# Kernel optimization log

Hardware: AMD Instinct MI355X
Metric: run time of the kernel (lower is better)

Reference implementation:

```python
import jax, jax.numpy as jnp
import numpy as np

N = 50000        # nodes
E = 640000       # edges
HID = 128        # hidden_channels
HEADS = 2
C = HID // 2     # out_channels per head (64)
ATT_SLOPE = 0.2  # GATv2Conv leaky_relu slope
OUT_SLOPE = 0.01 # F.leaky_relu default slope in GAT.forward


def setup_inputs() -> dict:
    key = jax.random.key(0)
    ks = jax.random.split(key, 11)
    s = 0.05
    return {
        "x": jax.random.normal(ks[0], (N, HID), dtype=jnp.float32),
        "edge_index": jax.random.randint(ks[1], (2, E), 0, N, dtype=jnp.int32),
        # layer 1 params (torch Linear layout: [out, in])
        "w_l1": jax.random.normal(ks[2], (HEADS * C, HID), dtype=jnp.float32) * s,
        "w_r1": jax.random.normal(ks[3], (HEADS * C, HID), dtype=jnp.float32) * s,
        "att1": jax.random.normal(ks[4], (HEADS, C), dtype=jnp.float32) * s,
        "b1": jnp.zeros((HEADS * C,), dtype=jnp.float32),
        # layer 2 params
        "w_l2": jax.random.normal(ks[5], (HEADS * C, HID), dtype=jnp.float32) * s,
        "w_r2": jax.random.normal(ks[6], (HEADS * C, HID), dtype=jnp.float32) * s,
        "att2": jax.random.normal(ks[7], (HEADS, C), dtype=jnp.float32) * s,
        "b2": jnp.zeros((HEADS * C,), dtype=jnp.float32),
    }


def gatv2_conv(x, src, dst, w_l, w_r, att, b):
    # x: [N, HID] -> out: [N, HEADS*C]  (concat=True), dropout inactive (eval)
    x_l = (x @ w_l.T).reshape(N, HEADS, C)  # source transform
    x_r = (x @ w_r.T).reshape(N, HEADS, C)  # target transform
    x_j = x_l[src]                           # [E, H, C] gathered source feats
    e = jax.nn.leaky_relu(x_j + x_r[dst], ATT_SLOPE)
    alpha = jnp.einsum('ehc,hc->eh', e, att)  # [E, H]
    # segment softmax over incoming edges of each target node
    amax = jax.ops.segment_max(alpha, dst, num_segments=N)
    amax = jnp.where(jnp.isfinite(amax), amax, 0.0)
    ex = jnp.exp(alpha - amax[dst])
    denom = jax.ops.segment_sum(ex, dst, num_segments=N)
    alpha = ex / (denom[dst] + 1e-16)
    out = jax.ops.segment_sum(alpha[:, :, None] * x_j, dst, num_segments=N)
    return out.reshape(N, HEADS * C) + b


def reference(x, edge_index, w_l1, w_r1, att1, b1, w_l2, w_r2, att2, b2):
    src, dst = edge_index[0], edge_index[1]
    h1 = jax.nn.leaky_relu(gatv2_conv(x, src, dst, w_l1, w_r1, att1, b1), OUT_SLOPE)
    h2 = gatv2_conv(h1, src, dst, w_l2, w_r2, att2, b2)
    return h1 + h2
```

## Files before the change

### kernel.cpp

```cpp
#include <hip/hip_runtime.h>
#include <hip/hip_bf16.h>
#include <cmath>

#define HID 128
#define ATT_SLOPE 0.2f
#define OUT_SLOPE 0.01f
#define LOG2E 1.44269504f
#define GM 64
#define ASTRIDE 144
#define CSRCAP 64

typedef __attribute__((ext_vector_type(8))) short bf16x8;
typedef __attribute__((ext_vector_type(4))) float f32x4;

__device__ __forceinline__ short f2bf(float f) {
    __hip_bfloat16 h = __float2bfloat16(f);
    return *reinterpret_cast<short*>(&h);
}
__device__ __forceinline__ unsigned packbf(float a, float b) {
    return (unsigned)(unsigned short)f2bf(a) | ((unsigned)(unsigned short)f2bf(b) << 16);
}
__device__ __forceinline__ float bflo(unsigned u) { return __uint_as_float(u << 16); }
__device__ __forceinline__ float bfhi(unsigned u) { return __uint_as_float(u & 0xffff0000u); }

__device__ __forceinline__ float fast_exp2(float x) {
#if __has_builtin(__builtin_amdgcn_exp2f)
    return __builtin_amdgcn_exp2f(x);
#else
    return exp2f(x);
#endif
}

__device__ __forceinline__ void gemm_tile(const float* __restrict__ X,
                                          const float* __restrict__ wl,
                                          const float* __restrict__ wr,
                                          unsigned* __restrict__ xlp,
                                          unsigned* __restrict__ xrp,
                                          int nNodes, int tile,
                                          short (*as)[ASTRIDE], int t) {
    int n0 = tile * GM;
    int w = t >> 6, lane = t & 63;
    int q = lane >> 4, ln = lane & 15;

    #pragma unroll
    for (int it = 0; it < 4; ++it) {
        int chunk = it * 256 + t;
        int r = chunk >> 4, c = chunk & 15;
        int gr = n0 + r;
        float4 u4 = make_float4(0.f, 0.f, 0.f, 0.f);
        float4 v4 = make_float4(0.f, 0.f, 0.f, 0.f);
        if (gr < nNodes) {
            const float4* pp = (const float4*)(X + (size_t)gr * HID + c * 8);
            u4 = pp[0]; v4 = pp[1];
        }
        bf16x8 b;
        b[0] = f2bf(u4.x); b[1] = f2bf(u4.y); b[2] = f2bf(u4.z); b[3] = f2bf(u4.w);
        b[4] = f2bf(v4.x); b[5] = f2bf(v4.y); b[6] = f2bf(v4.z); b[7] = f2bf(v4.w);
        *(bf16x8*)&as[r][c * 8] = b;
    }

    bf16x8 bfrag[4][4];
    #pragma unroll
    for (int ct = 0; ct < 4; ++ct) {
        int col = w * 64 + ct * 16 + ln;
        const float* Wp = (col < 128) ? (wl + (size_t)col * HID)
                                      : (wr + (size_t)(col - 128) * HID);
        #pragma unroll
        for (int ks = 0; ks < 4; ++ks) {
            const float4* pp = (const float4*)(Wp + ks * 32 + q * 8);
            float4 u4 = pp[0], v4 = pp[1];
            bf16x8 b;
            b[0] = f2bf(u4.x); b[1] = f2bf(u4.y); b[2] = f2bf(u4.z); b[3] = f2bf(u4.w);
            b[4] = f2bf(v4.x); b[5] = f2bf(v4.y); b[6] = f2bf(v4.z); b[7] = f2bf(v4.w);
            bfrag[ct][ks] = b;
        }
    }
    __syncthreads();

    f32x4 acc[4][4];
    #pragma unroll
    for (int rt = 0; rt < 4; ++rt)
        #pragma unroll
        for (int ct = 0; ct < 4; ++ct) acc[rt][ct] = (f32x4){0.f, 0.f, 0.f, 0.f};

    #pragma unroll
    for (int rt = 0; rt < 4; ++rt) {
        bf16x8 afrag[4];
        #pragma unroll
        for (int ks = 0; ks < 4; ++ks)
            afrag[ks] = *(const bf16x8*)&as[rt * 16 + ln][ks * 32 + q * 8];
        #pragma unroll
        for (int ks = 0; ks < 4; ++ks)
            #pragma unroll
            for (int ct = 0; ct < 4; ++ct)
                acc[rt][ct] = __builtin_amdgcn_mfma_f32_16x16x32_bf16(
                    afrag[ks], bfrag[ct][ks], acc[rt][ct], 0, 0, 0);
    }

    unsigned* dstp = (w < 2) ? xlp : xrp;
    int dbase = (w & 1) * 32 + ln;
    #pragma unroll
    for (int rt = 0; rt < 4; ++rt) {
        #pragma unroll
        for (int c2 = 0; c2 < 2; ++c2) {
            int d = dbase + c2 * 16;
            #pragma unroll
            for (int i = 0; i < 4; ++i) {
                int row = n0 + rt * 16 + q * 4 + i;
                if (row < nNodes)
                    dstp[(size_t)row * 64 + d] = packbf(acc[rt][c2][i], acc[rt][c2 + 2][i]);
            }
        }
    }
}

__global__ __launch_bounds__(256) void fused_g1_fill(const float* __restrict__ X,
                                                     const float* __restrict__ wl,
                                                     const float* __restrict__ wr,
                                                     unsigned* __restrict__ xlp,
                                                     unsigned* __restrict__ xrp,
                                                     const int* __restrict__ src,
                                                     const int* __restrict__ dst,
                                                     int* __restrict__ cnt,
                                                     int* __restrict__ csr,
                                                     int N, int E, int gtiles, int nblk) {
    __shared__ __align__(16) short as[GM][ASTRIDE];
    int bid = blockIdx.x, t = threadIdx.x;
    if (bid < gtiles) {
        gemm_tile(X, wl, wr, xlp, xrp, N, bid, as, t);
    } else {
        int stride = (nblk - gtiles) * 256;
        for (int e = (bid - gtiles) * 256 + t; e < E; e += stride) {
            int d = dst[e];
            int pos = atomicAdd(&cnt[d], 1);
            if (pos < CSRCAP) csr[(size_t)d * CSRCAP + pos] = src[e];
        }
    }
}

__global__ __launch_bounds__(256) void k_gemm(const float* __restrict__ X,
                                              const float* __restrict__ wl,
                                              const float* __restrict__ wr,
                                              unsigned* __restrict__ xlp,
                                              unsigned* __restrict__ xrp, int nNodes) {
    __shared__ __align__(16) short as[GM][ASTRIDE];
    gemm_tile(X, wl, wr, xlp, xrp, nNodes, blockIdx.x, as, threadIdx.x);
}

template <int LAYER>
__global__ __launch_bounds__(256) void gat_edge(const uint4* __restrict__ xlp4,
                                                const uint4* __restrict__ xrp4,
                                                const int* __restrict__ cnt,
                                                const int* __restrict__ csr,
                                                const float* __restrict__ att,
                                                const float* __restrict__ bias,
                                                const float* __restrict__ h1,
                                                float* __restrict__ outp, int nNodes) {
    int n = (int)((blockIdx.x * blockDim.x + threadIdx.x) >> 6);
    int lane = threadIdx.x & 63;
    if (n >= nNodes) return;
    const int slot = lane >> 4;
    const int u = lane & 15;
    const int lo_base = 4 * u + ((u < 8) ? 0 : 32);

    float a[8], asl[8];
    #pragma unroll
    for (int i = 0; i < 4; ++i) {
        a[2 * i]     = att[lo_base + i] * LOG2E;
        a[2 * i + 1] = att[lo_base + i + 32] * LOG2E;
        asl[2 * i]     = a[2 * i] * ATT_SLOPE;
        asl[2 * i + 1] = a[2 * i + 1] * ATT_SLOPE;
    }

    uint4 xrv = xrp4[(size_t)n * 16 + u];
    float xr8[8];
    {
        unsigned xv[4] = {xrv.x, xrv.y, xrv.z, xrv.w};
        #pragma unroll
        for (int i = 0; i < 4; ++i) { xr8[2 * i] = bflo(xv[i]); xr8[2 * i + 1] = bfhi(xv[i]); }
    }

    int dg = min(cnt[n], CSRCAP);
    const int* crow = csr + (size_t)n * CSRCAP;
    float l = 0.f, acc[8];
    #pragma unroll
    for (int i = 0; i < 8; ++i) acc[i] = 0.f;

    if (dg > 0) {
        int idx = lane < dg ? lane : dg - 1;
        int sreg = crow[idx];
        int rounds = (dg + 3) >> 2;
        for (int g = 0; g < rounds; ++g) {
            int j = g * 4 + slot;
            bool act = j < dg;
            int sj = min(j, dg - 1);
            int s = __shfl(sreg, sj, 64);
            uint4 v = xlp4[(size_t)s * 16 + u];
            unsigned xv[4] = {v.x, v.y, v.z, v.w};
            float x8[8];
            float pl = 0.f;
            #pragma unroll
            for (int i = 0; i < 4; ++i) {
                float xa = bflo(xv[i]), xb = bfhi(xv[i]);
                x8[2 * i] = xa; x8[2 * i + 1] = xb;
                float ta = xa + xr8[2 * i];
                float tb = xb + xr8[2 * i + 1];
                pl = fmaf(a[2 * i],       fmaxf(ta, 0.f), pl);
                pl = fmaf(asl[2 * i],     fminf(ta, 0.f), pl);
                pl = fmaf(a[2 * i + 1],   fmaxf(tb, 0.f), pl);
                pl = fmaf(asl[2 * i + 1], fminf(tb, 0.f), pl);
            }
            pl += __shfl_xor(pl, 1, 64);
            pl += __shfl_xor(pl, 2, 64);
            pl += __shfl_xor(pl, 4, 64);
            float wgt = act ? fast_exp2(pl) : 0.f;
            l += wgt;
            #pragma unroll
            for (int i = 0; i < 8; ++i) acc[i] = fmaf(wgt, x8[i], acc[i]);
        }
    }

    l += __shfl_xor(l, 32, 64);
    #pragma unroll
    for (int i = 0; i < 8; ++i) acc[i] += __shfl_xor(acc[i], 32, 64);
    l += __shfl_xor(l, 16, 64);
    #pragma unroll
    for (int i = 0; i < 8; ++i) acc[i] += __shfl_xor(acc[i], 16, 64);

    if (lane < 16) {
        size_t nb = (size_t)n * HID;
        float inv = 1.f / (l + 1e-16f);
        const float4 blo = *(const float4*)&bias[lo_base];
        const float4 bhi = *(const float4*)&bias[lo_base + 32];
        float o[8];
        o[0] = acc[0] * inv + blo.x; o[2] = acc[2] * inv + blo.y;
        o[4] = acc[4] * inv + blo.z; o[6] = acc[6] * inv + blo.w;
        o[1] = acc[1] * inv + bhi.x; o[3] = acc[3] * inv + bhi.y;
        o[5] = acc[5] * inv + bhi.z; o[7] = acc[7] * inv + bhi.w;
        if (LAYER == 1) {
            #pragma unroll
            for (int i = 0; i < 8; ++i) o[i] = o[i] > 0.f ? o[i] : OUT_SLOPE * o[i];
        } else {
            const float4 hlo = *(const float4*)&h1[nb + lo_base];
            const float4 hhi = *(const float4*)&h1[nb + lo_base + 32];
            o[0] += hlo.x; o[2] += hlo.y; o[4] += hlo.z; o[6] += hlo.w;
            o[1] += hhi.x; o[3] += hhi.y; o[5] += hhi.z; o[7] += hhi.w;
        }
        *(float4*)&outp[nb + lo_base]      = make_float4(o[0], o[2], o[4], o[6]);
        *(float4*)&outp[nb + lo_base + 32] = make_float4(o[1], o[3], o[5], o[7]);
    }
}

extern "C" void kernel_launch(void* const* d_in, const int* in_sizes, int n_in,
                              void* d_out, int out_size, void* d_ws, size_t ws_size,
                              hipStream_t stream) {
    const float* x    = (const float*)d_in[0];
    const int* ei     = (const int*)d_in[1];
    const float* w_l1 = (const float*)d_in[2];
    const float* w_r1 = (const float*)d_in[3];
    const float* att1 = (const float*)d_in[4];
    const float* b1   = (const float*)d_in[5];
    const float* w_l2 = (const float*)d_in[6];
    const float* w_r2 = (const float*)d_in[7];
    const float* att2 = (const float*)d_in[8];
    const float* b2   = (const float*)d_in[9];

    const int N = in_sizes[0] / HID;
    const int E = in_sizes[1] / 2;
    const int* srcp = ei;
    const int* dstp = ei + E;

    unsigned* xlp = (unsigned*)d_ws;
    unsigned* xrp = xlp + (size_t)N * 64;
    float* h1buf  = (float*)(xrp + (size_t)N * 64);
    int* cnt      = (int*)(h1buf + (size_t)N * HID);
    int* csr      = cnt + N;
    float* outf   = (float*)d_out;

    const int gtiles = (N + GM - 1) / GM;
    const int fillb  = (E + 255) / 256 / 2;
    const int nblk   = gtiles + fillb;
    const int ab     = (N + 3) / 4;

    hipMemsetAsync(cnt, 0, (size_t)N * sizeof(int), stream);
    fused_g1_fill<<<nblk, 256, 0, stream>>>(x, w_l1, w_r1, xlp, xrp,
                                            srcp, dstp, cnt, csr, N, E, gtiles, nblk);
    gat_edge<1><<<ab, 256, 0, stream>>>((const uint4*)xlp, (const uint4*)xrp,
                                        cnt, csr, att1, b1, nullptr, h1buf, N);
    k_gemm<<<gtiles, 256, 0, stream>>>(h1buf, w_l2, w_r2, xlp, xrp, N);
    gat_edge<2><<<ab, 256, 0, stream>>>((const uint4*)xlp, (const uint4*)xrp,
                                        cnt, csr, att2, b2, h1buf, outf, N);
}
```

Before: 241.9 us.

## Pad degree counters to 64B, batch CSR fill atomics, schedule fill blocks first

Each per-node degree counter now sits on its own 64-byte slot, so concurrent atomics on different nodes no longer contend on the same cache line. Fill threads now handle four edges each: all loads are issued first, then all atomics, then the stores, which gives more memory-level parallelism. Fill blocks are placed before the GEMM tiles in the grid so they are scheduled first. The trade-off is a 16x larger memset for the counters and a strided, less cache-friendly read of the counters in the edge kernels.

```diff
diff --git a/kernel.cpp b/kernel.cpp
--- a/kernel.cpp
+++ b/kernel.cpp
@@ -9,6 +9,7 @@
 #define GM 64
 #define ASTRIDE 144
 #define CSRCAP 64
+#define CNTSTRIDE 16
 
 typedef __attribute__((ext_vector_type(8))) short bf16x8;
 typedef __attribute__((ext_vector_type(4))) float f32x4;
@@ -123,18 +124,30 @@
                                                      const int* __restrict__ dst,
                                                      int* __restrict__ cnt,
                                                      int* __restrict__ csr,
-                                                     int N, int E, int gtiles, int nblk) {
+                                                     int N, int E, int fillb) {
     __shared__ __align__(16) short as[GM][ASTRIDE];
     int bid = blockIdx.x, t = threadIdx.x;
-    if (bid < gtiles) {
-        gemm_tile(X, wl, wr, xlp, xrp, N, bid, as, t);
+    if (bid >= fillb) {
+        gemm_tile(X, wl, wr, xlp, xrp, N, bid - fillb, as, t);
     } else {
-        int stride = (nblk - gtiles) * 256;
-        for (int e = (bid - gtiles) * 256 + t; e < E; e += stride) {
-            int d = dst[e];
-            int pos = atomicAdd(&cnt[d], 1);
-            if (pos < CSRCAP) csr[(size_t)d * CSRCAP + pos] = src[e];
-        }
+        int base = bid * 1024 + t;
+        int dd[4], ss[4];
+        bool v[4];
+        #pragma unroll
+        for (int i = 0; i < 4; ++i) {
+            int e = base + i * 256;
+            v[i] = e < E;
+            int ec = v[i] ? e : 0;
+            dd[i] = dst[ec];
+            ss[i] = src[ec];
+        }
+        int pp[4];
+        #pragma unroll
+        for (int i = 0; i < 4; ++i)
+            pp[i] = v[i] ? atomicAdd(&cnt[dd[i] << 4], 1) : CSRCAP;
+        #pragma unroll
+        for (int i = 0; i < 4; ++i)
+            if (pp[i] < CSRCAP) csr[(size_t)dd[i] * CSRCAP + pp[i]] = ss[i];
     }
 }
 
@@ -180,7 +193,7 @@
         for (int i = 0; i < 4; ++i) { xr8[2 * i] = bflo(xv[i]); xr8[2 * i + 1] = bfhi(xv[i]); }
     }
 
-    int dg = min(cnt[n], CSRCAP);
+    int dg = min(cnt[n << 4], CSRCAP);
     const int* crow = csr + (size_t)n * CSRCAP;
     float l = 0.f, acc[8];
     #pragma unroll
@@ -274,17 +287,17 @@
     unsigned* xrp = xlp + (size_t)N * 64;
     float* h1buf  = (float*)(xrp + (size_t)N * 64);
     int* cnt      = (int*)(h1buf + (size_t)N * HID);
-    int* csr      = cnt + N;
+    int* csr      = cnt + (size_t)N * CNTSTRIDE;
     float* outf   = (float*)d_out;
 
     const int gtiles = (N + GM - 1) / GM;
-    const int fillb  = (E + 255) / 256 / 2;
+    const int fillb  = (E + 1023) / 1024;
     const int nblk   = gtiles + fillb;
     const int ab     = (N + 3) / 4;
 
-    hipMemsetAsync(cnt, 0, (size_t)N * sizeof(int), stream);
+    hipMemsetAsync(cnt, 0, (size_t)N * CNTSTRIDE * sizeof(int), stream);
     fused_g1_fill<<<nblk, 256, 0, stream>>>(x, w_l1, w_r1, xlp, xrp,
-                                            srcp, dstp, cnt, csr, N, E, gtiles, nblk);
+                                            srcp, dstp, cnt, csr, N, E, fillb);
     gat_edge<1><<<ab, 256, 0, stream>>>((const uint4*)xlp, (const uint4*)xrp,
                                         cnt, csr, att1, b1, nullptr, h1buf, N);
     k_gemm<<<gtiles, 256, 0, stream>>>(h1buf, w_l2, w_r2, xlp, xrp, N);
```

Measured after the change: 236.8 us. -2.1%, faster.
